# Kernel optimization log

Hardware: AMD Instinct MI355X
Metric: run time of the kernel (lower is better)

The kernel has to match this reference:

```python
import jax, jax.numpy as jnp
import numpy as np

EPSILON = 1e-06

def setup_inputs() -> dict:
    key = jax.random.key(0)
    k1, k2, k3 = jax.random.split(key, 3)
    B, S, D = 4, 4096, 4096
    x = jax.random.normal(k1, (B, S, D), dtype=jnp.float32)
    residual = jax.random.normal(k2, (B, S, D), dtype=jnp.float32)
    gamma = jax.random.uniform(k3, (D,), dtype=jnp.float32)
    return {"x": x, "residual": residual, "gamma": gamma}

def reference(x, residual, gamma):
    # Pass 1: residual add + RMSNorm (row-wise over last dim)
    x_added = x + residual
    rstd = jax.lax.rsqrt(jnp.mean(jnp.square(x_added), axis=-1, keepdims=True) + EPSILON)
    output = x_added * rstd * gamma  # [B, S, D]
    # Pass 2: global abs-max dynamic int8 quantization
    max_val = jnp.max(jnp.abs(output))
    scale = max_val / 127.0
    q = jnp.clip(jnp.round(output / scale), -128, 127).astype(jnp.int8)
    return q
```

## Files before the change

### kernel.cpp

```cpp
#include <hip/hip_runtime.h>

#define DD 4096
#define NROWS 16384
#define EPS 1e-6f

typedef float fx4 __attribute__((ext_vector_type(4)));
typedef int   ix4 __attribute__((ext_vector_type(4)));


__global__ __launch_bounds__(256) void pass1(
    const float* __restrict__ x, const float* __restrict__ res,
    const float* __restrict__ gamma, unsigned int* __restrict__ outw,
    float* __restrict__ rowmax) {
  const int row = blockIdx.x;
  const int t = threadIdx.x;
  const fx4* x4 = (const fx4*)(x + (size_t)row * DD);
  const fx4* r4 = (const fx4*)(res + (size_t)row * DD);
  const fx4* g4 = (const fx4*)gamma;

  fx4 p[4];
  float ss = 0.f, mx = 0.f;
#pragma unroll
  for (int i = 0; i < 4; ++i) {
    const int idx = t + i * 256;
    fx4 y = x4[idx] + r4[idx];
    ss += y.x * y.x + y.y * y.y + y.z * y.z + y.w * y.w;
    p[i] = y * g4[idx];
    mx = fmaxf(mx, fmaxf(fmaxf(fabsf(p[i].x), fabsf(p[i].y)),
                         fmaxf(fabsf(p[i].z), fabsf(p[i].w))));
  }
#pragma unroll
  for (int off = 32; off > 0; off >>= 1) {
    ss += __shfl_down(ss, off, 64);
    mx = fmaxf(mx, __shfl_down(mx, off, 64));
  }
  __shared__ float s_ss[4], s_mx[4];
  const int wave = t >> 6, lane = t & 63;
  if (lane == 0) { s_ss[wave] = ss; s_mx[wave] = mx; }
  __syncthreads();
  const float tss = s_ss[0] + s_ss[1] + s_ss[2] + s_ss[3];
  const float tmx = fmaxf(fmaxf(s_mx[0], s_mx[1]), fmaxf(s_mx[2], s_mx[3]));
  const float rs = rsqrtf(tss * (1.0f / DD) + EPS);
  if (t == 0) rowmax[row] = tmx * rs;
  const float inv = tmx > 0.f ? 127.0f / tmx : 0.f;

  ix4 d;
  int* dp = (int*)&d;
#pragma unroll
  for (int i = 0; i < 4; ++i) {
    int a = min(max(__float2int_rn(p[i].x * inv), -127), 127);
    int b = min(max(__float2int_rn(p[i].y * inv), -127), 127);
    int c = min(max(__float2int_rn(p[i].z * inv), -127), 127);
    int e = min(max(__float2int_rn(p[i].w * inv), -127), 127);
    dp[i] = (a & 255) | ((b & 255) << 8) | ((c & 255) << 16) | ((e & 255) << 24);
  }
  *(ix4*)(outw + (size_t)row * DD + 4 * t) = d;
}

__global__ __launch_bounds__(1024) void reduce_gmax(
    const float* __restrict__ rowmax, float* __restrict__ gmax) {
  const int t = threadIdx.x;
  float m = 0.f;
#pragma unroll
  for (int i = 0; i < NROWS / 1024; ++i) m = fmaxf(m, rowmax[t + i * 1024]);
#pragma unroll
  for (int off = 32; off > 0; off >>= 1) m = fmaxf(m, __shfl_down(m, off, 64));
  __shared__ float s[16];
  if ((t & 63) == 0) s[t >> 6] = m;
  __syncthreads();
  if (t == 0) {
    float r = s[0];
#pragma unroll
    for (int i = 1; i < 16; ++i) r = fmaxf(r, s[i]);
    *gmax = r;
  }
}

__global__ __launch_bounds__(256) void pass2(
    unsigned int* __restrict__ outw, const float* __restrict__ rowmax,
    const float* __restrict__ gmax, int* __restrict__ out) {
  const int row = blockIdx.x;
  const int t = threadIdx.x;
  const float c = rowmax[row] / *gmax;
  union { ix4 v; unsigned int w[4]; } u;
  u.v = *(const ix4*)(outw + (size_t)row * DD + 4 * t);
  ix4* orow = (ix4*)(out + (size_t)row * DD);
#pragma unroll
  for (int i = 0; i < 4; ++i) {
    const unsigned int w = u.w[i];
    ix4 q;
    q.x = min(max(__float2int_rn((float)((int)(w << 24) >> 24) * c), -128), 127);
    q.y = min(max(__float2int_rn((float)((int)(w << 16) >> 24) * c), -128), 127);
    q.z = min(max(__float2int_rn((float)((int)(w << 8) >> 24) * c), -128), 127);
    q.w = min(max(__float2int_rn((float)((int)w >> 24) * c), -128), 127);
    orow[t + i * 256] = q;
  }
}

__global__ __launch_bounds__(256) void pass1_nb(
    const float* __restrict__ x, const float* __restrict__ res,
    const float* __restrict__ gamma, float* __restrict__ rstd,
    float* __restrict__ rowmax) {
  const int row = blockIdx.x;
  const int t = threadIdx.x;
  const fx4* x4 = (const fx4*)(x + (size_t)row * DD);
  const fx4* r4 = (const fx4*)(res + (size_t)row * DD);
  const fx4* g4 = (const fx4*)gamma;
  float ss = 0.f, mx = 0.f;
#pragma unroll
  for (int i = 0; i < 4; ++i) {
    const int idx = t + i * 256;
    fx4 y = x4[idx] + r4[idx];
    ss += y.x * y.x + y.y * y.y + y.z * y.z + y.w * y.w;
    fx4 p = y * g4[idx];
    mx = fmaxf(mx, fmaxf(fmaxf(fabsf(p.x), fabsf(p.y)),
                         fmaxf(fabsf(p.z), fabsf(p.w))));
  }
#pragma unroll
  for (int off = 32; off > 0; off >>= 1) {
    ss += __shfl_down(ss, off, 64);
    mx = fmaxf(mx, __shfl_down(mx, off, 64));
  }
  __shared__ float s_ss[4], s_mx[4];
  const int wave = t >> 6, lane = t & 63;
  if (lane == 0) { s_ss[wave] = ss; s_mx[wave] = mx; }
  __syncthreads();
  if (t == 0) {
    float tss = s_ss[0] + s_ss[1] + s_ss[2] + s_ss[3];
    float tmx = fmaxf(fmaxf(s_mx[0], s_mx[1]), fmaxf(s_mx[2], s_mx[3]));
    float rs = rsqrtf(tss * (1.0f / DD) + EPS);
    rstd[row] = rs;
    rowmax[row] = tmx * rs;
  }
}

__global__ __launch_bounds__(256) void pass2_nb(
    const float* __restrict__ x, const float* __restrict__ res,
    const float* __restrict__ gamma, const float* __restrict__ rstd,
    const float* __restrict__ gmax, int* __restrict__ out) {
  const int row = blockIdx.x;
  const int t = threadIdx.x;
  const float c = rstd[row] * (127.0f / *gmax);
  const fx4* x4 = (const fx4*)(x + (size_t)row * DD);
  const fx4* r4 = (const fx4*)(res + (size_t)row * DD);
  const fx4* g4 = (const fx4*)gamma;
  ix4* o4 = (ix4*)(out + (size_t)row * DD);
#pragma unroll
  for (int i = 0; i < 4; ++i) {
    const int idx = t + i * 256;
    fx4 xv = x4[idx], rv = r4[idx], gv = g4[idx];
    ix4 q;
    q.x = min(max(__float2int_rn((xv.x + rv.x) * gv.x * c), -128), 127);
    q.y = min(max(__float2int_rn((xv.y + rv.y) * gv.y * c), -128), 127);
    q.z = min(max(__float2int_rn((xv.z + rv.z) * gv.z * c), -128), 127);
    q.w = min(max(__float2int_rn((xv.w + rv.w) * gv.w * c), -128), 127);
    o4[idx] = q;
  }
}

extern "C" void kernel_launch(void* const* d_in, const int* in_sizes, int n_in,
                              void* d_out, int out_size, void* d_ws, size_t ws_size,
                              hipStream_t stream) {
  const float* x     = (const float*)d_in[0];
  const float* res   = (const float*)d_in[1];
  const float* gamma = (const float*)d_in[2];
  int* out = (int*)d_out;

  char* ws = (char*)d_ws;
  float* gmax   = (float*)ws;
  float* rowmax = (float*)(ws + 256);
  float* rstd   = (float*)(ws + 256 + 64 * 1024);

  if (ws_size >= (size_t)(2 << 20)) {
    unsigned int* outw = (unsigned int*)d_out;
    pass1<<<NROWS, 256, 0, stream>>>(x, res, gamma, outw, rowmax);
    reduce_gmax<<<1, 1024, 0, stream>>>(rowmax, gmax);
    pass2<<<NROWS, 256, 0, stream>>>(outw, rowmax, gmax, out);
  } else {
    pass1_nb<<<NROWS, 256, 0, stream>>>(x, res, gamma, rstd, rowmax);
    reduce_gmax<<<1, 1024, 0, stream>>>(rowmax, gmax);
    pass2_nb<<<NROWS, 256, 0, stream>>>(x, res, gamma, rstd, gmax, out);
  }
}
```

Measured before the change: 191.4 us.

## Split pass1 into producer/consumer warps with double-buffered fp16 LDS staging

Pass1 now processes 8 rows per block. Half the threads load x, residual and gamma and compute the row sums, staging the fp16-packed products in a double-buffered LDS area. The other half quantize the previous row from that buffer. The aim is to overlap the global loads with the quantize-and-store work. In exchange, only half the threads issue loads, a block barrier is added per row, and the fp16 intermediate can change rounding.

```diff
diff --git a/kernel.cpp b/kernel.cpp
--- a/kernel.cpp
+++ b/kernel.cpp
@@ -1,60 +1,93 @@
 #include <hip/hip_runtime.h>
+#include <hip/hip_fp16.h>
 
 #define DD 4096
 #define NROWS 16384
 #define EPS 1e-6f
+#define RPB 8
 
 typedef float fx4 __attribute__((ext_vector_type(4)));
 typedef int   ix4 __attribute__((ext_vector_type(4)));
 
-
-__global__ __launch_bounds__(256) void pass1(
+__global__ __launch_bounds__(256) void pass1_pc(
     const float* __restrict__ x, const float* __restrict__ res,
     const float* __restrict__ gamma, unsigned int* __restrict__ outw,
     float* __restrict__ rowmax) {
-  const int row = blockIdx.x;
-  const int t = threadIdx.x;
-  const fx4* x4 = (const fx4*)(x + (size_t)row * DD);
-  const fx4* r4 = (const fx4*)(res + (size_t)row * DD);
-  const fx4* g4 = (const fx4*)gamma;
-
-  fx4 p[4];
-  float ss = 0.f, mx = 0.f;
-#pragma unroll
-  for (int i = 0; i < 4; ++i) {
-    const int idx = t + i * 256;
-    fx4 y = x4[idx] + r4[idx];
-    ss += y.x * y.x + y.y * y.y + y.z * y.z + y.w * y.w;
-    p[i] = y * g4[idx];
-    mx = fmaxf(mx, fmaxf(fmaxf(fabsf(p[i].x), fabsf(p[i].y)),
-                         fmaxf(fabsf(p[i].z), fabsf(p[i].w))));
-  }
-#pragma unroll
-  for (int off = 32; off > 0; off >>= 1) {
-    ss += __shfl_down(ss, off, 64);
-    mx = fmaxf(mx, __shfl_down(mx, off, 64));
-  }
-  __shared__ float s_ss[4], s_mx[4];
-  const int wave = t >> 6, lane = t & 63;
-  if (lane == 0) { s_ss[wave] = ss; s_mx[wave] = mx; }
-  __syncthreads();
-  const float tss = s_ss[0] + s_ss[1] + s_ss[2] + s_ss[3];
-  const float tmx = fmaxf(fmaxf(s_mx[0], s_mx[1]), fmaxf(s_mx[2], s_mx[3]));
-  const float rs = rsqrtf(tss * (1.0f / DD) + EPS);
-  if (t == 0) rowmax[row] = tmx * rs;
-  const float inv = tmx > 0.f ? 127.0f / tmx : 0.f;
-
-  ix4 d;
-  int* dp = (int*)&d;
-#pragma unroll
-  for (int i = 0; i < 4; ++i) {
-    int a = min(max(__float2int_rn(p[i].x * inv), -127), 127);
-    int b = min(max(__float2int_rn(p[i].y * inv), -127), 127);
-    int c = min(max(__float2int_rn(p[i].z * inv), -127), 127);
-    int e = min(max(__float2int_rn(p[i].w * inv), -127), 127);
-    dp[i] = (a & 255) | ((b & 255) << 8) | ((c & 255) << 16) | ((e & 255) << 24);
-  }
-  *(ix4*)(outw + (size_t)row * DD + 4 * t) = d;
+  __shared__ unsigned long long ph[2][1024];
+  __shared__ float s_ss[2][2], s_mx[2][2];
+
+  const int tid = threadIdx.x;
+  const int base_row = blockIdx.x * RPB;
+
+  for (int k = 0; k <= RPB; ++k) {
+    if (tid < 128) {
+      if (k < RPB) {
+        const int row = base_row + k;
+        const fx4* x4 = (const fx4*)(x + (size_t)row * DD);
+        const fx4* r4 = (const fx4*)(res + (size_t)row * DD);
+        const fx4* g4 = (const fx4*)gamma;
+        unsigned long long* buf = ph[k & 1];
+        float ss = 0.f, mx = 0.f;
+#pragma unroll
+        for (int i = 0; i < 8; ++i) {
+          const int s = tid + i * 128;
+          fx4 y = x4[s] + r4[s];
+          ss += y.x * y.x + y.y * y.y + y.z * y.z + y.w * y.w;
+          fx4 p = y * g4[s];
+          mx = fmaxf(mx, fmaxf(fmaxf(fabsf(p.x), fabsf(p.y)),
+                               fmaxf(fabsf(p.z), fabsf(p.w))));
+          union { unsigned long long u; __half2 h2[2]; } pk_;
+          pk_.h2[0] = __floats2half2_rn(p.x, p.y);
+          pk_.h2[1] = __floats2half2_rn(p.z, p.w);
+          buf[s] = pk_.u;
+        }
+#pragma unroll
+        for (int off = 32; off > 0; off >>= 1) {
+          ss += __shfl_down(ss, off, 64);
+          mx = fmaxf(mx, __shfl_down(mx, off, 64));
+        }
+        if ((tid & 63) == 0) {
+          s_ss[k & 1][tid >> 6] = ss;
+          s_mx[k & 1][tid >> 6] = mx;
+        }
+      }
+    } else {
+      if (k > 0) {
+        const int row = base_row + k - 1;
+        const int c = tid - 128;
+        const int pb = (k - 1) & 1;
+        const float tss = s_ss[pb][0] + s_ss[pb][1];
+        const float tmx = fmaxf(s_mx[pb][0], s_mx[pb][1]);
+        const float rs = rsqrtf(tss * (1.0f / DD) + EPS);
+        if (c == 0) rowmax[row] = tmx * rs;
+        const float inv = tmx > 0.f ? 127.0f / tmx : 0.f;
+        const unsigned long long* buf = ph[pb];
+        unsigned int dw[8];
+#pragma unroll
+        for (int j = 0; j < 8; ++j) {
+          union { unsigned long long u; __half2 h2[2]; } v;
+          v.u = buf[c + j * 128];
+          float2 f0 = __half22float2(v.h2[0]);
+          float2 f1 = __half22float2(v.h2[1]);
+          int a = min(max(__float2int_rn(f0.x * inv), -127), 127);
+          int b = min(max(__float2int_rn(f0.y * inv), -127), 127);
+          int d = min(max(__float2int_rn(f1.x * inv), -127), 127);
+          int e = min(max(__float2int_rn(f1.y * inv), -127), 127);
+          dw[j] = (unsigned)(a & 255) | ((unsigned)(b & 255) << 8) |
+                  ((unsigned)(d & 255) << 16) | ((unsigned)(e & 255) << 24);
+        }
+        ix4 q0, q1;
+        ((int*)&q0)[0] = dw[0]; ((int*)&q0)[1] = dw[2];
+        ((int*)&q0)[2] = dw[4]; ((int*)&q0)[3] = dw[6];
+        ((int*)&q1)[0] = dw[1]; ((int*)&q1)[1] = dw[3];
+        ((int*)&q1)[2] = dw[5]; ((int*)&q1)[3] = dw[7];
+        unsigned int* qrow = outw + (size_t)row * DD;
+        *(ix4*)(qrow + 4 * c) = q0;
+        *(ix4*)(qrow + 4 * c + 512) = q1;
+      }
+    }
+    __syncthreads();
+  }
 }
 
 __global__ __launch_bounds__(1024) void reduce_gmax(
@@ -173,7 +206,7 @@
 
   if (ws_size >= (size_t)(2 << 20)) {
     unsigned int* outw = (unsigned int*)d_out;
-    pass1<<<NROWS, 256, 0, stream>>>(x, res, gamma, outw, rowmax);
+    pass1_pc<<<NROWS / RPB, 256, 0, stream>>>(x, res, gamma, outw, rowmax);
     reduce_gmax<<<1, 1024, 0, stream>>>(rowmax, gmax);
     pass2<<<NROWS, 256, 0, stream>>>(outw, rowmax, gmax, out);
   } else {
```

Result: slower. 206.0 us (+7.6%).

## Process each row with a single wave in a persistent pass1 grid

Applied to the files above, without the earlier changes.

Pass1 now maps one 64-lane wave to each row, and a grid of 512 blocks loops over 8 rows per wave. This removes the shared-memory cross-wave reduction and block barrier and uses xor shuffles instead. Each thread now holds 16 vectors of the row in registers, which raises register pressure and may lower occupancy in a bandwidth-bound kernel.

```diff
diff --git a/kernel.cpp b/kernel.cpp
--- a/kernel.cpp
+++ b/kernel.cpp
@@ -8,53 +8,60 @@
 typedef int   ix4 __attribute__((ext_vector_type(4)));
 
 
-__global__ __launch_bounds__(256) void pass1(
+__global__ __launch_bounds__(256) void pass1_pw(
     const float* __restrict__ x, const float* __restrict__ res,
     const float* __restrict__ gamma, unsigned int* __restrict__ outw,
     float* __restrict__ rowmax) {
-  const int row = blockIdx.x;
-  const int t = threadIdx.x;
-  const fx4* x4 = (const fx4*)(x + (size_t)row * DD);
-  const fx4* r4 = (const fx4*)(res + (size_t)row * DD);
+  const int wid = (int)(blockIdx.x << 2) | ((int)threadIdx.x >> 6);
+  const int l = threadIdx.x & 63;
   const fx4* g4 = (const fx4*)gamma;
 
-  fx4 p[4];
-  float ss = 0.f, mx = 0.f;
+  for (int k = 0; k < 8; ++k) {
+    const int row = wid + (k << 11);
+    const fx4* x4 = (const fx4*)(x + (size_t)row * DD);
+    const fx4* r4 = (const fx4*)(res + (size_t)row * DD);
+
+    fx4 p[4][4];
+    float ss = 0.f, mx = 0.f;
 #pragma unroll
-  for (int i = 0; i < 4; ++i) {
-    const int idx = t + i * 256;
-    fx4 y = x4[idx] + r4[idx];
-    ss += y.x * y.x + y.y * y.y + y.z * y.z + y.w * y.w;
-    p[i] = y * g4[idx];
-    mx = fmaxf(mx, fmaxf(fmaxf(fabsf(p[i].x), fabsf(p[i].y)),
-                         fmaxf(fabsf(p[i].z), fabsf(p[i].w))));
+    for (int s = 0; s < 4; ++s) {
+#pragma unroll
+      for (int i = 0; i < 4; ++i) {
+        const int a = 64 * s + l + 256 * i;
+        fx4 y = x4[a] + r4[a];
+        ss += y.x * y.x + y.y * y.y + y.z * y.z + y.w * y.w;
+        fx4 pv = y * g4[a];
+        p[s][i] = pv;
+        mx = fmaxf(mx, fmaxf(fmaxf(fabsf(pv.x), fabsf(pv.y)),
+                             fmaxf(fabsf(pv.z), fabsf(pv.w))));
+      }
+    }
+#pragma unroll
+    for (int off = 1; off < 64; off <<= 1) {
+      ss += __shfl_xor(ss, off, 64);
+      mx = fmaxf(mx, __shfl_xor(mx, off, 64));
+    }
+    const float rs = rsqrtf(ss * (1.0f / DD) + EPS);
+    if (l == 0) rowmax[row] = mx * rs;
+    const float inv = mx > 0.f ? 127.0f / mx : 0.f;
+
+    unsigned int* qrow = outw + (size_t)row * DD;
+#pragma unroll
+    for (int s = 0; s < 4; ++s) {
+      ix4 d;
+      int* dp = (int*)&d;
+#pragma unroll
+      for (int i = 0; i < 4; ++i) {
+        int a0 = min(max(__float2int_rn(p[s][i].x * inv), -127), 127);
+        int b0 = min(max(__float2int_rn(p[s][i].y * inv), -127), 127);
+        int c0 = min(max(__float2int_rn(p[s][i].z * inv), -127), 127);
+        int e0 = min(max(__float2int_rn(p[s][i].w * inv), -127), 127);
+        dp[i] = (a0 & 255) | ((b0 & 255) << 8) | ((c0 & 255) << 16) |
+                ((e0 & 255) << 24);
+      }
+      *(ix4*)(qrow + 4 * (64 * s + l)) = d;
+    }
   }
-#pragma unroll
-  for (int off = 32; off > 0; off >>= 1) {
-    ss += __shfl_down(ss, off, 64);
-    mx = fmaxf(mx, __shfl_down(mx, off, 64));
-  }
-  __shared__ float s_ss[4], s_mx[4];
-  const int wave = t >> 6, lane = t & 63;
-  if (lane == 0) { s_ss[wave] = ss; s_mx[wave] = mx; }
-  __syncthreads();
-  const float tss = s_ss[0] + s_ss[1] + s_ss[2] + s_ss[3];
-  const float tmx = fmaxf(fmaxf(s_mx[0], s_mx[1]), fmaxf(s_mx[2], s_mx[3]));
-  const float rs = rsqrtf(tss * (1.0f / DD) + EPS);
-  if (t == 0) rowmax[row] = tmx * rs;
-  const float inv = tmx > 0.f ? 127.0f / tmx : 0.f;
-
-  ix4 d;
-  int* dp = (int*)&d;
-#pragma unroll
-  for (int i = 0; i < 4; ++i) {
-    int a = min(max(__float2int_rn(p[i].x * inv), -127), 127);
-    int b = min(max(__float2int_rn(p[i].y * inv), -127), 127);
-    int c = min(max(__float2int_rn(p[i].z * inv), -127), 127);
-    int e = min(max(__float2int_rn(p[i].w * inv), -127), 127);
-    dp[i] = (a & 255) | ((b & 255) << 8) | ((c & 255) << 16) | ((e & 255) << 24);
-  }
-  *(ix4*)(outw + (size_t)row * DD + 4 * t) = d;
 }
 
 __global__ __launch_bounds__(1024) void reduce_gmax(
@@ -173,7 +180,7 @@
 
   if (ws_size >= (size_t)(2 << 20)) {
     unsigned int* outw = (unsigned int*)d_out;
-    pass1<<<NROWS, 256, 0, stream>>>(x, res, gamma, outw, rowmax);
+    pass1_pw<<<512, 256, 0, stream>>>(x, res, gamma, outw, rowmax);
     reduce_gmax<<<1, 1024, 0, stream>>>(rowmax, gmax);
     pass2<<<NROWS, 256, 0, stream>>>(outw, rowmax, gmax, out);
   } else {
```

After: 194.4 us. Within noise of the previous version (+1.5%).

## Fuse norm and global-max quantization into one cooperative kernel with grid sync

Applied to the files above, without the earlier changes.

Replaces the three-kernel path with a single cooperative kernel. Each block handles 16 rows and keeps the per-row packed int8 values in registers. The global abs-max is gathered with an atomicMax on the float bits, followed by a grid-wide sync, after which each block requantizes and writes the output. This removes the round trip of the packed intermediate through global memory plus two kernel launches. In exchange it adds a memset, an occupancy query on the host, heavy register pressure, and a strict read-then-write phase split with no overlap across the grid sync.

```diff
diff --git a/kernel.cpp b/kernel.cpp
--- a/kernel.cpp
+++ b/kernel.cpp
@@ -1,12 +1,96 @@
 #include <hip/hip_runtime.h>
+#include <hip/hip_cooperative_groups.h>
+
+namespace cg = cooperative_groups;
 
 #define DD 4096
 #define NROWS 16384
 #define EPS 1e-6f
+#define RPB 16
+#define CGRID (NROWS / RPB)
 
 typedef float fx4 __attribute__((ext_vector_type(4)));
 typedef int   ix4 __attribute__((ext_vector_type(4)));
 
+__global__ __launch_bounds__(256, 4) void fused_coop(
+    const float* __restrict__ x, const float* __restrict__ res,
+    const float* __restrict__ gamma, int* __restrict__ out,
+    unsigned int* __restrict__ gmax) {
+  const int t = threadIdx.x;
+  const int bid = blockIdx.x;
+  const fx4* g4 = (const fx4*)gamma;
+  __shared__ float s_ss[4], s_mx[4], s_g;
+
+  unsigned int q[RPB][4];
+  float rmx[RPB];
+  float bmax = 0.f;
+
+#pragma unroll
+  for (int r = 0; r < RPB; ++r) {
+    const int row = bid * RPB + r;
+    const fx4* x4 = (const fx4*)(x + (size_t)row * DD);
+    const fx4* r4 = (const fx4*)(res + (size_t)row * DD);
+    fx4 p[4];
+    float ss = 0.f, mx = 0.f;
+#pragma unroll
+    for (int i = 0; i < 4; ++i) {
+      const int idx = t + i * 256;
+      fx4 y = x4[idx] + r4[idx];
+      ss += y.x * y.x + y.y * y.y + y.z * y.z + y.w * y.w;
+      p[i] = y * g4[idx];
+      mx = fmaxf(mx, fmaxf(fmaxf(fabsf(p[i].x), fabsf(p[i].y)),
+                           fmaxf(fabsf(p[i].z), fabsf(p[i].w))));
+    }
+#pragma unroll
+    for (int off = 32; off > 0; off >>= 1) {
+      ss += __shfl_down(ss, off, 64);
+      mx = fmaxf(mx, __shfl_down(mx, off, 64));
+    }
+    if ((t & 63) == 0) { s_ss[t >> 6] = ss; s_mx[t >> 6] = mx; }
+    __syncthreads();
+    const float tss = s_ss[0] + s_ss[1] + s_ss[2] + s_ss[3];
+    const float tmx = fmaxf(fmaxf(s_mx[0], s_mx[1]), fmaxf(s_mx[2], s_mx[3]));
+    __syncthreads();
+    const float rs = rsqrtf(tss * (1.0f / DD) + EPS);
+    rmx[r] = tmx * rs;
+    bmax = fmaxf(bmax, rmx[r]);
+    const float inv = tmx > 0.f ? 127.0f / tmx : 0.f;
+#pragma unroll
+    for (int i = 0; i < 4; ++i) {
+      int a = min(max(__float2int_rn(p[i].x * inv), -127), 127);
+      int b = min(max(__float2int_rn(p[i].y * inv), -127), 127);
+      int c = min(max(__float2int_rn(p[i].z * inv), -127), 127);
+      int e = min(max(__float2int_rn(p[i].w * inv), -127), 127);
+      q[r][i] = (unsigned)(a & 255) | ((unsigned)(b & 255) << 8) |
+                ((unsigned)(c & 255) << 16) | ((unsigned)(e & 255) << 24);
+    }
+  }
+
+  if (t == 0) atomicMax(gmax, __float_as_uint(bmax));
+
+  cg::this_grid().sync();
+
+  if (t == 0) s_g = __uint_as_float(atomicMax(gmax, 0u));
+  __syncthreads();
+  const float g = s_g;
+
+#pragma unroll
+  for (int r = 0; r < RPB; ++r) {
+    const int row = bid * RPB + r;
+    ix4* orow = (ix4*)(out + (size_t)row * DD);
+    const float c = rmx[r] / g;
+#pragma unroll
+    for (int i = 0; i < 4; ++i) {
+      const unsigned w = q[r][i];
+      ix4 o;
+      o.x = min(max(__float2int_rn((float)((int)(w << 24) >> 24) * c), -128), 127);
+      o.y = min(max(__float2int_rn((float)((int)(w << 16) >> 24) * c), -128), 127);
+      o.z = min(max(__float2int_rn((float)((int)(w << 8) >> 24) * c), -128), 127);
+      o.w = min(max(__float2int_rn((float)((int)w >> 24) * c), -128), 127);
+      orow[t + i * 256] = o;
+    }
+  }
+}
 
 __global__ __launch_bounds__(256) void pass1(
     const float* __restrict__ x, const float* __restrict__ res,
@@ -58,7 +142,7 @@
 }
 
 __global__ __launch_bounds__(1024) void reduce_gmax(
-    const float* __restrict__ rowmax, float* __restrict__ gmax) {
+    const float* __restrict__ rowmax, float* __restrict__ gmaxf) {
   const int t = threadIdx.x;
   float m = 0.f;
 #pragma unroll
@@ -72,16 +156,16 @@
     float r = s[0];
 #pragma unroll
     for (int i = 1; i < 16; ++i) r = fmaxf(r, s[i]);
-    *gmax = r;
+    *gmaxf = r;
   }
 }
 
 __global__ __launch_bounds__(256) void pass2(
     unsigned int* __restrict__ outw, const float* __restrict__ rowmax,
-    const float* __restrict__ gmax, int* __restrict__ out) {
+    const float* __restrict__ gmaxf, int* __restrict__ out) {
   const int row = blockIdx.x;
   const int t = threadIdx.x;
-  const float c = rowmax[row] / *gmax;
+  const float c = rowmax[row] / *gmaxf;
   union { ix4 v; unsigned int w[4]; } u;
   u.v = *(const ix4*)(outw + (size_t)row * DD + 4 * t);
   ix4* orow = (ix4*)(out + (size_t)row * DD);
@@ -97,67 +181,6 @@
   }
 }
 
-__global__ __launch_bounds__(256) void pass1_nb(
-    const float* __restrict__ x, const float* __restrict__ res,
-    const float* __restrict__ gamma, float* __restrict__ rstd,
-    float* __restrict__ rowmax) {
-  const int row = blockIdx.x;
-  const int t = threadIdx.x;
-  const fx4* x4 = (const fx4*)(x + (size_t)row * DD);
-  const fx4* r4 = (const fx4*)(res + (size_t)row * DD);
-  const fx4* g4 = (const fx4*)gamma;
-  float ss = 0.f, mx = 0.f;
-#pragma unroll
-  for (int i = 0; i < 4; ++i) {
-    const int idx = t + i * 256;
-    fx4 y = x4[idx] + r4[idx];
-    ss += y.x * y.x + y.y * y.y + y.z * y.z + y.w * y.w;
-    fx4 p = y * g4[idx];
-    mx = fmaxf(mx, fmaxf(fmaxf(fabsf(p.x), fabsf(p.y)),
-                         fmaxf(fabsf(p.z), fabsf(p.w))));
-  }
-#pragma unroll
-  for (int off = 32; off > 0; off >>= 1) {
-    ss += __shfl_down(ss, off, 64);
-    mx = fmaxf(mx, __shfl_down(mx, off, 64));
-  }
-  __shared__ float s_ss[4], s_mx[4];
-  const int wave = t >> 6, lane = t & 63;
-  if (lane == 0) { s_ss[wave] = ss; s_mx[wave] = mx; }
-  __syncthreads();
-  if (t == 0) {
-    float tss = s_ss[0] + s_ss[1] + s_ss[2] + s_ss[3];
-    float tmx = fmaxf(fmaxf(s_mx[0], s_mx[1]), fmaxf(s_mx[2], s_mx[3]));
-    float rs = rsqrtf(tss * (1.0f / DD) + EPS);
-    rstd[row] = rs;
-    rowmax[row] = tmx * rs;
-  }
-}
-
-__global__ __launch_bounds__(256) void pass2_nb(
-    const float* __restrict__ x, const float* __restrict__ res,
-    const float* __restrict__ gamma, const float* __restrict__ rstd,
-    const float* __restrict__ gmax, int* __restrict__ out) {
-  const int row = blockIdx.x;
-  const int t = threadIdx.x;
-  const float c = rstd[row] * (127.0f / *gmax);
-  const fx4* x4 = (const fx4*)(x + (size_t)row * DD);
-  const fx4* r4 = (const fx4*)(res + (size_t)row * DD);
-  const fx4* g4 = (const fx4*)gamma;
-  ix4* o4 = (ix4*)(out + (size_t)row * DD);
-#pragma unroll
-  for (int i = 0; i < 4; ++i) {
-    const int idx = t + i * 256;
-    fx4 xv = x4[idx], rv = r4[idx], gv = g4[idx];
-    ix4 q;
-    q.x = min(max(__float2int_rn((xv.x + rv.x) * gv.x * c), -128), 127);
-    q.y = min(max(__float2int_rn((xv.y + rv.y) * gv.y * c), -128), 127);
-    q.z = min(max(__float2int_rn((xv.z + rv.z) * gv.z * c), -128), 127);
-    q.w = min(max(__float2int_rn((xv.w + rv.w) * gv.w * c), -128), 127);
-    o4[idx] = q;
-  }
-}
-
 extern "C" void kernel_launch(void* const* d_in, const int* in_sizes, int n_in,
                               void* d_out, int out_size, void* d_ws, size_t ws_size,
                               hipStream_t stream) {
@@ -167,18 +190,23 @@
   int* out = (int*)d_out;
 
   char* ws = (char*)d_ws;
-  float* gmax   = (float*)ws;
+  unsigned int* gmax_u = (unsigned int*)ws;
+  float* gmax_f = (float*)ws;
   float* rowmax = (float*)(ws + 256);
-  float* rstd   = (float*)(ws + 256 + 64 * 1024);
-
-  if (ws_size >= (size_t)(2 << 20)) {
+
+  int occ = 0;
+  hipOccupancyMaxActiveBlocksPerMultiprocessor(&occ, fused_coop, 256, 0);
+
+  if (occ >= 4 && ws_size >= (size_t)(1 << 20)) {
+    hipMemsetAsync(d_ws, 0, 4, stream);
+    void* args[] = {(void*)&x, (void*)&res, (void*)&gamma,
+                    (void*)&out, (void*)&gmax_u};
+    hipLaunchCooperativeKernel((void*)fused_coop, dim3(CGRID), dim3(256),
+                               args, 0, stream);
+  } else {
     unsigned int* outw = (unsigned int*)d_out;
     pass1<<<NROWS, 256, 0, stream>>>(x, res, gamma, outw, rowmax);
-    reduce_gmax<<<1, 1024, 0, stream>>>(rowmax, gmax);
-    pass2<<<NROWS, 256, 0, stream>>>(outw, rowmax, gmax, out);
-  } else {
-    pass1_nb<<<NROWS, 256, 0, stream>>>(x, res, gamma, rstd, rowmax);
-    reduce_gmax<<<1, 1024, 0, stream>>>(rowmax, gmax);
-    pass2_nb<<<NROWS, 256, 0, stream>>>(x, res, gamma, rstd, gmax, out);
-  }
-}
+    reduce_gmax<<<1, 1024, 0, stream>>>(rowmax, gmax_f);
+    pass2<<<NROWS, 256, 0, stream>>>(outw, rowmax, gmax_f, out);
+  }
+}
```

New measurement: 191.2 us. No clear change (-0.1%).
